# Kernel optimization log

Hardware: AMD Instinct MI355X
Metric: run time of the kernel (lower is better)

The kernel has to match this reference:

```python
import jax, jax.numpy as jnp
import numpy as np
import math

N_NODES = 16384
N_GRAPHS = 512
E2 = 65536
E3 = 393216
EMB = 300
SCH = 128
NG = 50
CUTOFF = 10.0
NL_GIN = 5
NL_SCH = 6
NTASK = 12


def _ssp(x):
    # ShiftedSoftplus used by SchNet
    return jax.nn.softplus(x) - math.log(2.0)


def _seg(x, ids, n):
    return jax.ops.segment_sum(x, ids, num_segments=n)


def _forward(x2d, edge_index_2d, edge_attr_2d, batch, z, pos, edge_index_3d,
             atom_emb1, atom_emb2, vn_init,
             gin_W1, gin_b1, gin_W2, gin_b2, gin_bond1, gin_bond2, gin_gamma, gin_beta,
             vn_W1, vn_b1, vn_W2, vn_b2,
             sch_emb, s_mW1, s_mb1, s_mW2, s_mb2, s_lin1W, s_lin2W, s_lin2b, s_linW, s_linb,
             p2W, p2b, p3W, p3b, gW1, gb1, gW2, gb2, cW1, cb1, cW2, cb2):
    counts = jnp.maximum(_seg(jnp.ones((N_NODES,), jnp.float32), batch, N_GRAPHS), 1.0)[:, None]
    # ---------- GIN (2D) encoder with virtual node (OGB-style, eval mode: dropout off, BN uses running stats 0/1) ----------
    src2, dst2 = edge_index_2d[0], edge_index_2d[1]
    h = atom_emb1[x2d[:, 0]] + atom_emb2[x2d[:, 1]]              # [N, 300]
    vn = jnp.broadcast_to(vn_init, (N_GRAPHS, EMB))
    for l in range(NL_GIN):
        h_in = h + vn[batch]
        eemb = gin_bond1[l][edge_attr_2d[:, 0]] + gin_bond2[l][edge_attr_2d[:, 1]]
        msg = jax.nn.relu(h_in[src2] + eemb)                     # [E2, 300]
        agg = _seg(msg, dst2, N_NODES)
        t = jax.nn.relu((h_in + agg) @ gin_W1[l] + gin_b1[l]) @ gin_W2[l] + gin_b2[l]
        t = t * gin_gamma[l] + gin_beta[l]                       # eval-mode BatchNorm
        if l < NL_GIN - 1:
            t = jax.nn.relu(t)
            vn_tmp = _seg(t, batch, N_GRAPHS) + vn
            vn = jax.nn.relu(jax.nn.relu(vn_tmp @ vn_W1[l] + vn_b1[l]) @ vn_W2[l] + vn_b2[l])
        h = t
    h2d = _seg(h, batch, N_GRAPHS) / counts                      # global_mean_pool
    # ---------- SchNet (3D) encoder: interaction layers only, residual additions ----------
    src3, dst3 = edge_index_3d[0], edge_index_3d[1]
    diff = pos[dst3] - pos[src3]
    d = jnp.sqrt(jnp.sum(diff * diff, axis=-1))                  # edge_weight [E3]; no self loops -> d > 0
    offsets = jnp.linspace(0.0, CUTOFF, NG)
    coeff = -0.5 / (offsets[1] - offsets[0]) ** 2
    rbf = jnp.exp(coeff * (d[:, None] - offsets) ** 2)           # GaussianSmearing [E3, 50]
    C = 0.5 * (jnp.cos(d * math.pi / CUTOFF) + 1.0)              # cosine cutoff
    hs = sch_emb[z]                                              # [N, 128]
    for l in range(NL_SCH):
        Wf = (_ssp(rbf @ s_mW1[l] + s_mb1[l]) @ s_mW2[l] + s_mb2[l]) * C[:, None]  # filter net [E3, 128]
        x1 = hs @ s_lin1W[l]                                     # CFConv lin1 (no bias)
        agg = _seg(x1[src3] * Wf, dst3, N_NODES)                 # continuous-filter conv
        x2 = agg @ s_lin2W[l] + s_lin2b[l]                       # CFConv lin2
        hs = hs + (_ssp(x2) @ s_linW[l] + s_linb[l])             # block act+lin, residual
    h3d = _seg(hs, batch, N_GRAPHS) / counts
    # ---------- gated fusion + classifier (dropout off in eval) ----------
    h2p = h2d @ p2W + p2b
    h3p = h3d @ p3W + p3b
    g = jax.nn.sigmoid(jax.nn.relu(jnp.concatenate([h2p, h3p], axis=1) @ gW1 + gb1) @ gW2 + gb2)  # [B, 1]
    hf = g * h2p + (1.0 - g) * h3p
    return jax.nn.relu(hf @ cW1 + cb1) @ cW2 + cb2               # [N_GRAPHS, NTASK]


def setup_inputs() -> dict:
    key = jax.random.key(0)
    ks = jax.random.split(key, 40)
    def r(i, shape, s=0.02):
        return jax.random.normal(ks[i], shape, dtype=jnp.float32) * s
    x2d = jax.random.randint(ks[0], (N_NODES, 2), 0, 3)
    src2 = jax.random.randint(ks[1], (E2,), 0, N_NODES)
    dst2 = (src2 + jax.random.randint(ks[2], (E2,), 1, N_NODES)) % N_NODES  # no self loops
    edge_index_2d = jnp.stack([src2, dst2])
    edge_attr_2d = jax.random.randint(ks[3], (E2, 2), 0, 3)
    batch = jnp.sort(jax.random.randint(ks[4], (N_NODES,), 0, N_GRAPHS))
    z = jax.random.randint(ks[5], (N_NODES,), 0, 100)
    pos = jax.random.normal(ks[6], (N_NODES, 3), dtype=jnp.float32) * 2.0
    src3 = jax.random.randint(ks[7], (E3,), 0, N_NODES)
    dst3 = (src3 + jax.random.randint(ks[8], (E3,), 1, N_NODES)) % N_NODES
    edge_index_3d = jnp.stack([src3, dst3])
    return dict(
        x2d=x2d, edge_index_2d=edge_index_2d, edge_attr_2d=edge_attr_2d, batch=batch,
        z=z, pos=pos, edge_index_3d=edge_index_3d,
        atom_emb1=r(9, (120, EMB)), atom_emb2=r(10, (3, EMB)),
        vn_init=jnp.zeros((EMB,), jnp.float32),
        gin_W1=r(11, (NL_GIN, EMB, 2 * EMB)), gin_b1=jnp.zeros((NL_GIN, 2 * EMB), jnp.float32),
        gin_W2=r(12, (NL_GIN, 2 * EMB, EMB)), gin_b2=jnp.zeros((NL_GIN, EMB), jnp.float32),
        gin_bond1=r(13, (NL_GIN, 6, EMB)), gin_bond2=r(14, (NL_GIN, 3, EMB)),
        gin_gamma=jnp.ones((NL_GIN, EMB), jnp.float32), gin_beta=jnp.zeros((NL_GIN, EMB), jnp.float32),
        vn_W1=r(15, (NL_GIN - 1, EMB, 2 * EMB)), vn_b1=jnp.zeros((NL_GIN - 1, 2 * EMB), jnp.float32),
        vn_W2=r(16, (NL_GIN - 1, 2 * EMB, EMB)), vn_b2=jnp.zeros((NL_GIN - 1, EMB), jnp.float32),
        sch_emb=r(17, (100, SCH), 0.1),
        s_mW1=r(18, (NL_SCH, NG, SCH), 0.1), s_mb1=jnp.zeros((NL_SCH, SCH), jnp.float32),
        s_mW2=r(19, (NL_SCH, SCH, SCH), 0.1), s_mb2=jnp.zeros((NL_SCH, SCH), jnp.float32),
        s_lin1W=r(20, (NL_SCH, SCH, SCH), 0.1),
        s_lin2W=r(21, (NL_SCH, SCH, SCH), 0.1), s_lin2b=jnp.zeros((NL_SCH, SCH), jnp.float32),
        s_linW=r(22, (NL_SCH, SCH, SCH), 0.1), s_linb=jnp.zeros((NL_SCH, SCH), jnp.float32),
        p2W=r(23, (EMB, EMB)), p2b=jnp.zeros((EMB,), jnp.float32),
        p3W=r(24, (SCH, EMB)), p3b=jnp.zeros((EMB,), jnp.float32),
        gW1=r(25, (2 * EMB, 128)), gb1=jnp.zeros((128,), jnp.float32),
        gW2=r(26, (128, 1)), gb2=jnp.zeros((1,), jnp.float32),
        cW1=r(27, (EMB, EMB // 2)), cb1=jnp.zeros((EMB // 2,), jnp.float32),
        cW2=r(28, (EMB // 2, NTASK)), cb2=jnp.zeros((NTASK,), jnp.float32),
    )


def reference(x2d, edge_index_2d, edge_attr_2d, batch, z, pos, edge_index_3d,
              atom_emb1, atom_emb2, vn_init,
              gin_W1, gin_b1, gin_W2, gin_b2, gin_bond1, gin_bond2, gin_gamma, gin_beta,
              vn_W1, vn_b1, vn_W2, vn_b2,
              sch_emb, s_mW1, s_mb1, s_mW2, s_mb2, s_lin1W, s_lin2W, s_lin2b, s_linW, s_linb,
              p2W, p2b, p3W, p3b, gW1, gb1, gW2, gb2, cW1, cb1, cW2, cb2):
    return _forward(x2d, edge_index_2d, edge_attr_2d, batch, z, pos, edge_index_3d,
                    atom_emb1, atom_emb2, vn_init,
                    gin_W1, gin_b1, gin_W2, gin_b2, gin_bond1, gin_bond2, gin_gamma, gin_beta,
                    vn_W1, vn_b1, vn_W2, vn_b2,
                    sch_emb, s_mW1, s_mb1, s_mW2, s_mb2, s_lin1W, s_lin2W, s_lin2b, s_linW, s_linb,
                    p2W, p2b, p3W, p3b, gW1, gb1, gW2, gb2, cW1, cb1, cW2, cb2)
```

## Files before the change

### kernel.cpp

```cpp
#include <hip/hip_runtime.h>
#include <hip/hip_bf16.h>
#include <math.h>

#define NN 16384
#define NG 512
#define NE2 65536
#define NE3 393216
#define DEMB 300
#define DSCH 128
#define NRBF 50
#define NTAB 5120
#define TROWS 5121
#define DMAX 25.0f

typedef __attribute__((ext_vector_type(8))) short bf16x8;
typedef __attribute__((ext_vector_type(4))) float f32x4;

__device__ __forceinline__ float sspf(float x) {
  float sp = log1pf(expf(-fabsf(x))) + fmaxf(x, 0.f);
  return sp - 0.69314718055994530942f;
}

__device__ __forceinline__ short f2b(float f) {
  union { float f; unsigned u; } v;
  v.f = f;
  unsigned r = v.u + 0x7FFF + ((v.u >> 16) & 1);
  return (short)(r >> 16);
}

__device__ __forceinline__ float b2f(unsigned short b) {
  union { unsigned u; float f; } v;
  v.u = ((unsigned)b) << 16;
  return v.f;
}


__global__ void k_hist3(const int* __restrict__ ei2, const int* __restrict__ ei3,
                        const int* __restrict__ batch, int* __restrict__ cnt2,
                        int* __restrict__ cnt3, int* __restrict__ cntg) {
  int i = blockIdx.x * blockDim.x + threadIdx.x;
  if (i < NE2) {
    atomicAdd(&cnt2[ei2[NE2 + i]], 1);
  } else if (i < NE2 + NE3) {
    atomicAdd(&cnt3[ei3[NE3 + (i - NE2)]], 1);
  } else if (i < NE2 + NE3 + NN) {
    atomicAdd(&cntg[batch[i - NE2 - NE3]], 1);
  }
}

__global__ __launch_bounds__(1024) void k_scan3(const int* __restrict__ c0, int* __restrict__ o0,
                                                int n0, const int* __restrict__ c1,
                                                int* __restrict__ o1, int n1,
                                                const int* __restrict__ c2, int* __restrict__ o2,
                                                int n2) {
  const int* cnt = (blockIdx.x == 0) ? c0 : (blockIdx.x == 1) ? c1 : c2;
  int* off = (blockIdx.x == 0) ? o0 : (blockIdx.x == 1) ? o1 : o2;
  int n = (blockIdx.x == 0) ? n0 : (blockIdx.x == 1) ? n1 : n2;
  __shared__ int part[1024];
  int tid = threadIdx.x;
  int per = (n + 1023) / 1024;
  int base = tid * per;
  int sum = 0;
  for (int i = 0; i < per; ++i) {
    int idx = base + i;
    if (idx < n) sum += cnt[idx];
  }
  part[tid] = sum;
  __syncthreads();
  for (int d = 1; d < 1024; d <<= 1) {
    int v = (tid >= d) ? part[tid - d] : 0;
    __syncthreads();
    part[tid] += v;
    __syncthreads();
  }
  int run = (tid == 0) ? 0 : part[tid - 1];
  for (int i = 0; i < per; ++i) {
    int idx = base + i;
    if (idx < n) {
      off[idx] = run;
      run += cnt[idx];
    }
  }
  if (tid == 0) off[n] = part[1023];
}

__global__ void k_scatterB(const int* __restrict__ ei2, const int* __restrict__ ea2,
                           const int* __restrict__ batch, const int* __restrict__ off2,
                           int* __restrict__ cur2, int* __restrict__ s2s, int* __restrict__ ec2s,
                           int* __restrict__ b2s, const int* __restrict__ ei3,
                           const float* __restrict__ pos, const int* __restrict__ off3,
                           int* __restrict__ cur3, int* __restrict__ s3s, int* __restrict__ id3s,
                           float* __restrict__ fr3s) {
  int i = blockIdx.x * blockDim.x + threadIdx.x;
  if (i < NE2) {
    int e = i;
    int s = ei2[e], d = ei2[NE2 + e];
    int p = atomicAdd(&cur2[d], 1);
    int j = off2[d] + p;
    s2s[j] = s;
    ec2s[j] = ea2[2 * e] * 4 + ea2[2 * e + 1];
    b2s[j] = batch[s];
  } else if (i < NE2 + NE3) {
    int e = i - NE2;
    int s = ei3[e], d = ei3[NE3 + e];
    float dx = pos[3 * d] - pos[3 * s];
    float dy = pos[3 * d + 1] - pos[3 * s + 1];
    float dz = pos[3 * d + 2] - pos[3 * s + 2];
    float dist = sqrtf(dx * dx + dy * dy + dz * dz);
    float u = fminf(dist * ((float)NTAB / DMAX), (float)NTAB - 0.001f);
    int idx = (int)u;
    int p = atomicAdd(&cur3[d], 1);
    int j = off3[d] + p;
    s3s[j] = s;
    id3s[j] = idx;
    fr3s[j] = u - (float)idx;
  }
}


__global__ void k_init_gin(const int* __restrict__ x2d, const float* __restrict__ e1,
                           const float* __restrict__ e2, short* __restrict__ hb,
                           const float* __restrict__ vni, float* __restrict__ vn,
                           short* __restrict__ vnb) {
  int i = blockIdx.x * blockDim.x + threadIdx.x;
  if (i < NN * DEMB) {
    int n = i / DEMB, c = i - n * DEMB;
    hb[i] = f2b(e1[x2d[2 * n] * DEMB + c] + e2[x2d[2 * n + 1] * DEMB + c]);
  } else if (i < NN * DEMB + NG * DEMB) {
    int j = i - NN * DEMB;
    float v = vni[j % DEMB];
    vn[j] = v;
    vnb[j] = f2b(v);
  }
}

__global__ void k_init_sch(float* __restrict__ rbs, float* __restrict__ Cs,
                           const int* __restrict__ z, const float* __restrict__ emb,
                           float* __restrict__ hs, short* __restrict__ hsb) {
  int i = blockIdx.x * blockDim.x + threadIdx.x;
  if (i < TROWS * NRBF) {
    int j = i / NRBF, k = i - j * NRBF;
    float dj = (float)j * (DMAX / (float)NTAB);
    const float step = 10.0f / 49.0f;
    const float coeff = -0.5f / (step * step);
    float t = dj - (float)k * step;
    rbs[i] = expf(coeff * t * t);
    if (k == 0) Cs[j] = 0.5f * (cosf(dj * (3.14159265358979323846f / 10.0f)) + 1.0f);
  } else if (i < TROWS * NRBF + NN * DSCH) {
    int j = i - TROWS * NRBF;
    float v = emb[z[j >> 7] * DSCH + (j & 127)];
    hs[j] = v;
    hsb[j] = f2b(v);
  }
}

__global__ __launch_bounds__(256) void k_head5(
    const float* __restrict__ h2d, const float* __restrict__ h3d, const float* __restrict__ p2W,
    const float* __restrict__ p2b, const float* __restrict__ p3W, const float* __restrict__ p3b,
    const float* __restrict__ gW1, const float* __restrict__ gb1, const float* __restrict__ gW2,
    const float* __restrict__ gb2, const float* __restrict__ cW1, const float* __restrict__ cb1,
    const float* __restrict__ cW2, const float* __restrict__ cb2, float* __restrict__ out) {
  __shared__ float sx[DEMB], sy[DSCH], h2p[DEMB], h3p[DEMB], ghl[DSCH], c1l[150];
  __shared__ float pa[2][128], pb[2][128];
  __shared__ float gshare;
  int g = blockIdx.x, tid = threadIdx.x;
  int half = tid >> 7, o7 = tid & 127;
  for (int i = tid; i < DEMB; i += 256) sx[i] = h2d[(size_t)g * DEMB + i];
  if (tid < DSCH) sy[tid] = h3d[(size_t)g * DSCH + tid];
  __syncthreads();
  for (int ob = 0; ob < DEMB; ob += 128) {
    int o = ob + o7;
    float a0 = 0.f, a1 = 0.f, b0 = 0.f, b1 = 0.f;
    if (o < DEMB) {
      int kb = half * 150;
      for (int k = kb; k < kb + 150; k += 2) {
        a0 = fmaf(sx[k], p2W[k * 300 + o], a0);
        a1 = fmaf(sx[k + 1], p2W[(k + 1) * 300 + o], a1);
      }
      int kb3 = half * 64;
      for (int k = kb3; k < kb3 + 64; k += 2) {
        b0 = fmaf(sy[k], p3W[k * 300 + o], b0);
        b1 = fmaf(sy[k + 1], p3W[(k + 1) * 300 + o], b1);
      }
    }
    pa[half][o7] = a0 + a1;
    pb[half][o7] = b0 + b1;
    __syncthreads();
    if (half == 0 && o < DEMB) {
      h2p[o] = pa[0][o7] + pa[1][o7] + p2b[o];
      h3p[o] = pb[0][o7] + pb[1][o7] + p3b[o];
    }
    __syncthreads();
  }
  {
    const float* src = (half == 0) ? h2p : h3p;
    const float* wb = gW1 + (half ? 300 * 128 : 0);
    float a0 = 0.f, a1 = 0.f, a2 = 0.f, a3 = 0.f;
    for (int k = 0; k < 300; k += 4) {
      a0 = fmaf(src[k], wb[k * 128 + o7], a0);
      a1 = fmaf(src[k + 1], wb[(k + 1) * 128 + o7], a1);
      a2 = fmaf(src[k + 2], wb[(k + 2) * 128 + o7], a2);
      a3 = fmaf(src[k + 3], wb[(k + 3) * 128 + o7], a3);
    }
    pa[half][o7] = (a0 + a1) + (a2 + a3);
    __syncthreads();
    if (half == 0) ghl[o7] = fmaxf(pa[0][o7] + pa[1][o7] + gb1[o7], 0.f);
    __syncthreads();
  }
  if (tid < 128) pa[0][tid] = ghl[tid] * gW2[tid];
  __syncthreads();
  for (int s = 64; s > 0; s >>= 1) {
    if (tid < s) pa[0][tid] += pa[0][tid + s];
    __syncthreads();
  }
  if (tid == 0) gshare = 1.0f / (1.0f + expf(-(pa[0][0] + gb2[0])));
  __syncthreads();
  float gg = gshare;
  for (int i = tid; i < DEMB; i += 256) sx[i] = gg * h2p[i] + (1.0f - gg) * h3p[i];
  __syncthreads();
  for (int ob = 0; ob < 150; ob += 128) {
    int o = ob + o7;
    float a0 = 0.f, a1 = 0.f;
    if (o < 150) {
      int kb = half * 150;
      for (int k = kb; k < kb + 150; k += 2) {
        a0 = fmaf(sx[k], cW1[k * 150 + o], a0);
        a1 = fmaf(sx[k + 1], cW1[(k + 1) * 150 + o], a1);
      }
    }
    pa[half][o7] = a0 + a1;
    __syncthreads();
    if (half == 0 && o < 150) c1l[o] = fmaxf(pa[0][o7] + pa[1][o7] + cb1[o], 0.f);
    __syncthreads();
  }
  if (tid < 12) {
    float a = cb2[tid];
    for (int k = 0; k < 150; ++k) a = fmaf(c1l[k], cW2[k * 12 + tid], a);
    out[(size_t)g * 12 + tid] = a;
  }
}


__global__ __launch_bounds__(256) void k_gin_gather4(
    const short* __restrict__ hb, const short* __restrict__ vnb, const int* __restrict__ batch,
    const int* __restrict__ off2, const int* __restrict__ s2s, const int* __restrict__ ec2s,
    const int* __restrict__ b2s, const float* __restrict__ bond1,
    const float* __restrict__ bond2, short* __restrict__ aggb) {
  __shared__ float sb[9 * DEMB];
  int tid = threadIdx.x;
  for (int i = tid; i < 6 * DEMB; i += 256) sb[i] = bond1[i];
  for (int i = tid; i < 3 * DEMB; i += 256) sb[6 * DEMB + i] = bond2[i];
  __syncthreads();
  int d = blockIdx.x * 4 + (tid >> 6);
  int lane = tid & 63;
  int j0 = off2[d], j1 = off2[d + 1];
  const unsigned short* hd = (const unsigned short*)hb + (size_t)d * DEMB;
  const unsigned short* vd = (const unsigned short*)vnb + (size_t)batch[d] * DEMB;
  float acc[5];
#pragma unroll
  for (int q = 0; q < 5; ++q) {
    int col = lane + 64 * q;
    acc[q] = (col < DEMB) ? b2f(hd[col]) + b2f(vd[col]) : 0.f;
  }
  for (int j = j0; j < j1; ++j) {
    int s = s2s[j], ec = ec2s[j], bs = b2s[j];
    const unsigned short* hr = (const unsigned short*)hb + (size_t)s * DEMB;
    const unsigned short* vr = (const unsigned short*)vnb + (size_t)bs * DEMB;
    const float* b1 = sb + (ec >> 2) * DEMB;
    const float* b2 = sb + 6 * DEMB + (ec & 3) * DEMB;
#pragma unroll
    for (int q = 0; q < 5; ++q) {
      int col = lane + 64 * q;
      if (col < DEMB) acc[q] += fmaxf(b2f(hr[col]) + b2f(vr[col]) + b1[col] + b2[col], 0.f);
    }
  }
  short* outr = aggb + (size_t)d * 320;
#pragma unroll
  for (int q = 0; q < 5; ++q) {
    int col = lane + 64 * q;
    outr[col] = (col < DEMB) ? f2b(acc[q]) : (short)0;
  }
}

__global__ __launch_bounds__(256) void k_conv_gather4(
    const short* __restrict__ ftabb, const short* __restrict__ x1b, const int* __restrict__ off3,
    const int* __restrict__ s3s, const int* __restrict__ id3s, const float* __restrict__ fr3s,
    short* __restrict__ agg3b) {
  int tid = threadIdx.x;
  int d = blockIdx.x * 4 + (tid >> 6);
  int lane = tid & 63;
  int j0 = off3[d], j1 = off3[d + 1];
  float a0 = 0.f, a1 = 0.f;
  for (int j = j0; j < j1; ++j) {
    int s = s3s[j], idx = id3s[j];
    float fr = fr3s[j];
    unsigned t0 = ((const unsigned*)(ftabb + (size_t)idx * 128))[lane];
    unsigned t1 = ((const unsigned*)(ftabb + (size_t)(idx + 1) * 128))[lane];
    unsigned xv = ((const unsigned*)(x1b + (size_t)s * 128))[lane];
    float t0a = b2f((unsigned short)(t0 & 0xFFFF)), t0b = b2f((unsigned short)(t0 >> 16));
    float t1a = b2f((unsigned short)(t1 & 0xFFFF)), t1b = b2f((unsigned short)(t1 >> 16));
    a0 += (t0a + fr * (t1a - t0a)) * b2f((unsigned short)(xv & 0xFFFF));
    a1 += (t0b + fr * (t1b - t0b)) * b2f((unsigned short)(xv >> 16));
  }
  unsigned pack = ((unsigned)(unsigned short)f2b(a1) << 16) | (unsigned short)f2b(a0);
  ((unsigned*)(agg3b + (size_t)d * 128))[lane] = pack;
}

__global__ __launch_bounds__(256) void k_poolb300(const short* __restrict__ xb,
                                                  const int* __restrict__ goff,
                                                  float* __restrict__ out) {
  int g = blockIdx.x * 4 + (threadIdx.x >> 6);
  int lane = threadIdx.x & 63;
  if (g >= NG) return;
  int r0 = goff[g], r1 = goff[g + 1];
  float acc[5] = {};
  for (int r = r0; r < r1; ++r) {
    const unsigned short* row = (const unsigned short*)xb + (size_t)r * DEMB;
#pragma unroll
    for (int q = 0; q < 5; ++q) {
      int col = lane + 64 * q;
      if (col < DEMB) acc[q] += b2f(row[col]);
    }
  }
  float s = 1.0f / fmaxf((float)(r1 - r0), 1.0f);
#pragma unroll
  for (int q = 0; q < 5; ++q) {
    int col = lane + 64 * q;
    if (col < DEMB) out[(size_t)g * DEMB + col] = acc[q] * s;
  }
}

__global__ __launch_bounds__(256) void k_poolb128(const short* __restrict__ xb,
                                                  const int* __restrict__ goff,
                                                  float* __restrict__ out) {
  int g = blockIdx.x * 4 + (threadIdx.x >> 6);
  int lane = threadIdx.x & 63;
  if (g >= NG) return;
  int r0 = goff[g], r1 = goff[g + 1];
  float a0 = 0.f, a1 = 0.f;
  for (int r = r0; r < r1; ++r) {
    unsigned v = ((const unsigned*)(xb + (size_t)r * DSCH))[lane];
    a0 += b2f((unsigned short)(v & 0xFFFF));
    a1 += b2f((unsigned short)(v >> 16));
  }
  float s = 1.0f / fmaxf((float)(r1 - r0), 1.0f);
  out[(size_t)g * DSCH + lane * 2] = a0 * s;
  out[(size_t)g * DSCH + lane * 2 + 1] = a1 * s;
}

__global__ __launch_bounds__(256) void k_poolvn(const short* __restrict__ hb,
                                                const int* __restrict__ goff,
                                                const float* __restrict__ vn,
                                                short* __restrict__ vnab) {
  int g = blockIdx.x * 4 + (threadIdx.x >> 6);
  int lane = threadIdx.x & 63;
  if (g >= NG) return;
  int r0 = goff[g], r1 = goff[g + 1];
  float acc[5] = {};
  for (int r = r0; r < r1; ++r) {
    const unsigned short* row = (const unsigned short*)hb + (size_t)r * DEMB;
#pragma unroll
    for (int q = 0; q < 5; ++q) {
      int col = lane + 64 * q;
      if (col < DEMB) acc[q] += b2f(row[col]);
    }
  }
  short* outr = vnab + (size_t)g * 320;
#pragma unroll
  for (int q = 0; q < 5; ++q) {
    int col = lane + 64 * q;
    if (col < 320)
      outr[col] = (col < DEMB) ? f2b(acc[q] + vn[(size_t)g * DEMB + col]) : (short)0;
  }
}

__global__ void k_prepw2(const float* __restrict__ Wa, const float* __restrict__ Wb,
                         short* __restrict__ Wta, short* __restrict__ Wtb, int K, int N, int Kp,
                         int Np, int La, int Lb) {
  int i = blockIdx.x * blockDim.x + threadIdx.x;
  int per = Np * Kp;
  if (i >= (La + Lb) * per) return;
  int l = i / per, r = i - l * per;
  int n = r / Kp, k = r - n * Kp;
  const float* W = (l < La) ? Wa : Wb;
  int ll = (l < La) ? l : l - La;
  short* Wt = (l < La) ? Wta : Wtb;
  float v = (n < N && k < K) ? W[(size_t)ll * K * N + (size_t)k * N + n] : 0.f;
  Wt[(size_t)ll * per + r] = f2b(v);
}

__global__ void k_prepw3(const float* __restrict__ W0, const float* __restrict__ W1,
                         const float* __restrict__ W2, short* __restrict__ T0,
                         short* __restrict__ T1, short* __restrict__ T2) {
  int i = blockIdx.x * blockDim.x + threadIdx.x;
  const int per = 6 * 128 * 128;
  if (i >= 3 * per) return;
  int which = i / per, r = i - which * per;
  int l = r / 16384, rr = r - l * 16384;
  int n = rr / 128, k = rr - n * 128;
  const float* W = (which == 0) ? W0 : (which == 1) ? W1 : W2;
  short* T = (which == 0) ? T0 : (which == 1) ? T1 : T2;
  T[r] = f2b(W[(size_t)l * 16384 + (size_t)k * 128 + n]);
}

template <int ACT>
__global__ __launch_bounds__(256) void k_gemmz(
    const float* __restrict__ A, const float* __restrict__ B, const float* __restrict__ bias,
    const float* __restrict__ rscale, float* __restrict__ Cout, short* __restrict__ Coutb,
    int M, int N, int K, int ldc, long strideA, long strideB, long strideBias, long strideC) {
  A += (size_t)blockIdx.z * strideA;
  B += (size_t)blockIdx.z * strideB;
  bias += (size_t)blockIdx.z * strideBias;
  __shared__ float sA[16][65];
  __shared__ float sB[16][64];
  int tid = threadIdx.x;
  int tx = tid & 15, ty = tid >> 4;
  int bm = blockIdx.y * 64, bn = blockIdx.x * 64;
  float acc[4][4] = {};
  for (int k0 = 0; k0 < K; k0 += 16) {
#pragma unroll
    for (int t = 0; t < 4; ++t) {
      int i = tid + t * 256;
      int m = i >> 4, kk = i & 15;
      int gm = bm + m, gk = k0 + kk;
      sA[kk][m] = (gm < M && gk < K) ? A[(size_t)gm * K + gk] : 0.f;
    }
#pragma unroll
    for (int t = 0; t < 4; ++t) {
      int i = tid + t * 256;
      int kk = i >> 6, n = i & 63;
      int gk = k0 + kk, gn = bn + n;
      sB[kk][n] = (gk < K && gn < N) ? B[(size_t)gk * N + gn] : 0.f;
    }
    __syncthreads();
#pragma unroll
    for (int kk = 0; kk < 16; ++kk) {
      float a[4], b[4];
#pragma unroll
      for (int i = 0; i < 4; ++i) a[i] = sA[kk][ty + 16 * i];
#pragma unroll
      for (int j = 0; j < 4; ++j) b[j] = sB[kk][tx + 16 * j];
#pragma unroll
      for (int i = 0; i < 4; ++i)
#pragma unroll
        for (int j = 0; j < 4; ++j) acc[i][j] = fmaf(a[i], b[j], acc[i][j]);
    }
    __syncthreads();
  }
#pragma unroll
  for (int i = 0; i < 4; ++i) {
    int gm = bm + ty + 16 * i;
    if (gm >= M) continue;
    float rs = rscale ? rscale[gm] : 1.0f;
#pragma unroll
    for (int j = 0; j < 4; ++j) {
      int gn = bn + tx + 16 * j;
      if (gn >= N) continue;
      float v = acc[i][j] + bias[gn];
      if (ACT == 1) v = fmaxf(v, 0.f);
      if (ACT == 2) v = sspf(v);
      v *= rs;
      if (Cout) Cout[(size_t)blockIdx.z * strideC + (size_t)gm * ldc + gn] = v;
      if (Coutb) Coutb[(size_t)blockIdx.z * strideC + (size_t)gm * ldc + gn] = f2b(v);
    }
  }
}

template <int ACT>
__global__ __launch_bounds__(256) void k_mgemm_bf(
    const short* __restrict__ Ab, const short* __restrict__ Wt, const float* __restrict__ bias,
    const float* __restrict__ scale, const float* __restrict__ shift,
    const float* __restrict__ Cin, float* __restrict__ Cout, short* __restrict__ Coutb,
    int M, int N, int Kp, int ldc, int ldcb, int Nb) {
  __shared__ short sA[128 * 32];
  const int tid = threadIdx.x;
  const int lane = tid & 63;
  const int w = tid >> 6;
  const int wm = w >> 1, wn = w & 1;
  const int bm = blockIdx.y * 128, bn = blockIdx.x * 128;

  f32x4 acc[4][4] = {};

  const int sr = tid >> 1;
  const int sk = (tid & 1) * 16;
  const short* Arow = Ab + (size_t)(bm + sr) * Kp + sk;
// ... 304 lines not shown
                              int out_size, void* d_ws, size_t ws_size, hipStream_t stream) {
  const int* x2d = (const int*)d_in[0];
  const int* ei2 = (const int*)d_in[1];
  const int* ea2 = (const int*)d_in[2];
  const int* batch = (const int*)d_in[3];
  const int* z = (const int*)d_in[4];
  const float* pos = (const float*)d_in[5];
  const int* ei3 = (const int*)d_in[6];
  const float* atom_emb1 = (const float*)d_in[7];
  const float* atom_emb2 = (const float*)d_in[8];
  const float* vn_init = (const float*)d_in[9];
  const float* gin_W1 = (const float*)d_in[10];
  const float* gin_b1 = (const float*)d_in[11];
  const float* gin_W2 = (const float*)d_in[12];
  const float* gin_b2 = (const float*)d_in[13];
  const float* gin_bond1 = (const float*)d_in[14];
  const float* gin_bond2 = (const float*)d_in[15];
  const float* gin_gamma = (const float*)d_in[16];
  const float* gin_beta = (const float*)d_in[17];
  const float* vn_W1 = (const float*)d_in[18];
  const float* vn_b1 = (const float*)d_in[19];
  const float* vn_W2 = (const float*)d_in[20];
  const float* vn_b2 = (const float*)d_in[21];
  const float* sch_emb = (const float*)d_in[22];
  const float* s_mW1 = (const float*)d_in[23];
  const float* s_mb1 = (const float*)d_in[24];
  const float* s_mW2 = (const float*)d_in[25];
  const float* s_mb2 = (const float*)d_in[26];
  const float* s_lin1W = (const float*)d_in[27];
  const float* s_lin2W = (const float*)d_in[28];
  const float* s_lin2b = (const float*)d_in[29];
  const float* s_linW = (const float*)d_in[30];
  const float* s_linb = (const float*)d_in[31];
  const float* p2W = (const float*)d_in[32];
  const float* p2b = (const float*)d_in[33];
  const float* p3W = (const float*)d_in[34];
  const float* p3b = (const float*)d_in[35];
  const float* gW1 = (const float*)d_in[36];
  const float* gb1 = (const float*)d_in[37];
  const float* gW2 = (const float*)d_in[38];
  const float* gb2 = (const float*)d_in[39];
  const float* cW1 = (const float*)d_in[40];
  const float* cb1 = (const float*)d_in[41];
  const float* cW2 = (const float*)d_in[42];
  const float* cb2 = (const float*)d_in[43];

  float* ws = (float*)d_ws;
  short* hb = (short*)ws;
  int* b2s = (int*)(ws + 2500000);
  short* aggb = (short*)(ws + 5000000);
  short* y1b = (short*)(ws + 7700000);
  float* rbs = ws + 400000;
  float* Cs = ws + 700000;
  float* t1all = ws + 800000;
  short* ftabb = (short*)(ws + 4800000);
  float* hs = ws + 8800000;
  short* x1b = (short*)(ws + 11000000);
  short* agg3b = (short*)(ws + 13200000);
  short* hsb = (short*)(ws + 15400000);
  short* W1t = (short*)(ws + 20000000);
  short* W2t = (short*)(ws + 20600000);
  short* s1t = (short*)(ws + 21200000);
  short* s2t = (short*)(ws + 21300000);
  short* s3t = (short*)(ws + 21400000);
  int* I = (int*)(ws + 22000000);
  int* cnt2 = I + 0;
  int* cnt3 = I + 16384;
  int* cntg = I + 32768;
  int* cur2 = I + 33280;
  int* cur3 = I + 49664;
  int* off2 = I + 70000;
  int* off3 = I + 90000;
  int* goff = I + 110000;
  int* s2s = I + 120000;
  int* ec2s = I + 190000;
  int* s3s = I + 260000;
  int* id3s = I + 660000;
  float* fr3s = (float*)(I + 1060000);
  short* vnW1t = (short*)(ws + 23500000);
  short* vnW2t = (short*)(ws + 24000000);
  short* vnab = (short*)(ws + 24500000);
  short* vnhb = (short*)(ws + 24600000);
  short* vnb = (short*)(ws + 24800000);
  float* vn = ws + 28443136;
  float* h2d = ws + 29057536;
  float* h3d = ws + 29211136;

  k_prepw2<<<(9 * 640 * 320 + 255) / 256, 256, 0, stream>>>(gin_W1, vn_W1, W1t, vnW1t, 300, 600,
                                                            320, 640, 5, 4);
  k_prepw2<<<(9 * 384 * 608 + 255) / 256, 256, 0, stream>>>(gin_W2, vn_W2, W2t, vnW2t, 600, 300,
                                                            608, 384, 5, 4);
  k_prepw3<<<(3 * 6 * 16384 + 255) / 256, 256, 0, stream>>>(s_lin1W, s_lin2W, s_linW, s1t, s2t,
                                                            s3t);

  hipMemsetAsync(I, 0, 66048 * sizeof(int), stream);
  k_hist3<<<(NE2 + NE3 + NN + 255) / 256, 256, 0, stream>>>(ei2, ei3, batch, cnt2, cnt3, cntg);
  k_scan3<<<3, 1024, 0, stream>>>(cnt2, off2, 16384, cnt3, off3, 16384, cntg, goff, 512);
  k_scatterB<<<(NE2 + NE3 + 255) / 256, 256, 0, stream>>>(ei2, ea2, batch, off2, cur2, s2s, ec2s,
                                                          b2s, ei3, pos, off3, cur3, s3s, id3s,
                                                          fr3s);

  k_init_gin<<<(NN * DEMB + NG * DEMB + 255) / 256, 256, 0, stream>>>(x2d, atom_emb1, atom_emb2,
                                                                      hb, vn_init, vn, vnb);
  for (int l = 0; l < 5; ++l) {
    k_gin_gather4<<<NN / 4, 256, 0, stream>>>(hb, vnb, batch, off2, s2s, ec2s, b2s,
                                              gin_bond1 + l * 6 * DEMB, gin_bond2 + l * 3 * DEMB,
                                              aggb);
    run_mgemm_bf(stream, aggb, W1t + (size_t)l * 640 * 320, gin_b1 + l * 600, nullptr, nullptr,
                 nullptr, nullptr, y1b, NN, 600, 320, 0, 608, 608, 1);
    run_mgemm_bf(stream, y1b, W2t + (size_t)l * 384 * 608, gin_b2 + l * 300, gin_gamma + l * 300,
                 gin_beta + l * 300, nullptr, nullptr, hb, NN, 300, 608, 0, 300, 300,
                 (l < 4) ? 1 : 0);
    if (l < 4) {
      k_poolvn<<<NG / 4, 256, 0, stream>>>(hb, goff, vn, vnab);
      run_mgemm_bf64(stream, vnab, vnW1t + (size_t)l * 640 * 320, vn_b1 + l * 600, nullptr,
                     nullptr, nullptr, nullptr, vnhb, NG, 600, 320, 0, 608, 608, 1);
      run_mgemm_bf64(stream, vnhb, vnW2t + (size_t)l * 384 * 608, vn_b2 + l * 300, nullptr,
                     nullptr, nullptr, vn, vnb, NG, 300, 608, 300, 300, 300, 1);
    }
  }
  k_poolb300<<<NG / 4, 256, 0, stream>>>(hb, goff, h2d);

  k_init_sch<<<(TROWS * NRBF + NN * DSCH + 255) / 256, 256, 0, stream>>>(rbs, Cs, z, sch_emb, hs,
                                                                         hsb);
  {
    dim3 ga(2, (TROWS + 63) / 64, 6);
    k_gemmz<2><<<ga, 256, 0, stream>>>(rbs, s_mW1, s_mb1, nullptr, t1all, nullptr, TROWS, 128, 50,
                                       128, 0L, 50L * 128, 128L, (long)TROWS * 128);
    k_gemmz<0><<<ga, 256, 0, stream>>>(t1all, s_mW2, s_mb2, Cs, nullptr, ftabb, TROWS, 128, 128,
                                       128, (long)TROWS * 128, 128L * 128, 128L,
                                       (long)TROWS * 128);
  }
  run_mgemm_bf64(stream, hsb, s1t, nullptr, nullptr, nullptr, nullptr, nullptr, x1b, NN, 128, 128,
                 0, 128, 128, 0);
  for (int l = 0; l < 6; ++l) {
    k_conv_gather4<<<NN / 4, 256, 0, stream>>>(ftabb + (size_t)l * TROWS * 128, x1b, off3, s3s,
                                               id3s, fr3s, agg3b);
    if (l < 5)
      k_sch_fused<0><<<NN / 64, 256, 0, stream>>>(agg3b, s2t + (size_t)l * 16384,
                                                  s_lin2b + l * 128, s3t + (size_t)l * 16384,
                                                  s_linb + l * 128, s1t + (size_t)(l + 1) * 16384,
                                                  hs, hsb, x1b);
    else
      k_sch_fused<1><<<NN / 64, 256, 0, stream>>>(agg3b, s2t + (size_t)l * 16384,
                                                  s_lin2b + l * 128, s3t + (size_t)l * 16384,
                                                  s_linb + l * 128, s1t, hs, hsb, x1b);
  }
  k_poolb128<<<NG / 4, 256, 0, stream>>>(hsb, goff, h3d);

  k_head5<<<NG, 256, 0, stream>>>(h2d, h3d, p2W, p2b, p3W, p3b, gW1, gb1, gW2, gb2, cW1, cb1, cW2,
                                  cb2, (float*)d_out);
}
```

Before: 1.349 ms.

## Replace scalar head kernel with bf16 matrix GEMMs and vectorize gathers

The per-graph scalar head kernel is replaced by a chain of bf16 matrix-core GEMMs over concatenated, padded weight matrices, with a small blend kernel for the gate. Pooling now writes bf16 into a shared concatenated input buffer. Separately, the GIN gather is rewritten to load packed bf16 pairs as 32-bit words and to pre-sum the two bond embeddings into a combined bf16 table in shared memory. This adds bf16 rounding of head weights and bond sums, plus an extra weight-prep launch.

```diff
diff --git a/kernel.cpp b/kernel.cpp
--- a/kernel.cpp
+++ b/kernel.cpp
@@ -32,6 +32,10 @@
   union { unsigned u; float f; } v;
   v.u = ((unsigned)b) << 16;
   return v.f;
+}
+
+__device__ __forceinline__ unsigned pk2(float a, float b) {
+  return ((unsigned)(unsigned short)f2b(b) << 16) | (unsigned short)f2b(a);
 }
 
 
@@ -154,132 +158,69 @@
   }
 }
 
-__global__ __launch_bounds__(256) void k_head5(
-    const float* __restrict__ h2d, const float* __restrict__ h3d, const float* __restrict__ p2W,
-    const float* __restrict__ p2b, const float* __restrict__ p3W, const float* __restrict__ p3b,
-    const float* __restrict__ gW1, const float* __restrict__ gb1, const float* __restrict__ gW2,
-    const float* __restrict__ gb2, const float* __restrict__ cW1, const float* __restrict__ cb1,
-    const float* __restrict__ cW2, const float* __restrict__ cb2, float* __restrict__ out) {
-  __shared__ float sx[DEMB], sy[DSCH], h2p[DEMB], h3p[DEMB], ghl[DSCH], c1l[150];
-  __shared__ float pa[2][128], pb[2][128];
-  __shared__ float gshare;
-  int g = blockIdx.x, tid = threadIdx.x;
-  int half = tid >> 7, o7 = tid & 127;
-  for (int i = tid; i < DEMB; i += 256) sx[i] = h2d[(size_t)g * DEMB + i];
-  if (tid < DSCH) sy[tid] = h3d[(size_t)g * DSCH + tid];
-  __syncthreads();
-  for (int ob = 0; ob < DEMB; ob += 128) {
-    int o = ob + o7;
-    float a0 = 0.f, a1 = 0.f, b0 = 0.f, b1 = 0.f;
-    if (o < DEMB) {
-      int kb = half * 150;
-      for (int k = kb; k < kb + 150; k += 2) {
-        a0 = fmaf(sx[k], p2W[k * 300 + o], a0);
-        a1 = fmaf(sx[k + 1], p2W[(k + 1) * 300 + o], a1);
-      }
-      int kb3 = half * 64;
-      for (int k = kb3; k < kb3 + 64; k += 2) {
-        b0 = fmaf(sy[k], p3W[k * 300 + o], b0);
-        b1 = fmaf(sy[k + 1], p3W[(k + 1) * 300 + o], b1);
-      }
-    }
-    pa[half][o7] = a0 + a1;
-    pb[half][o7] = b0 + b1;
-    __syncthreads();
-    if (half == 0 && o < DEMB) {
-      h2p[o] = pa[0][o7] + pa[1][o7] + p2b[o];
-      h3p[o] = pb[0][o7] + pb[1][o7] + p3b[o];
-    }
-    __syncthreads();
-  }
-  {
-    const float* src = (half == 0) ? h2p : h3p;
-    const float* wb = gW1 + (half ? 300 * 128 : 0);
-    float a0 = 0.f, a1 = 0.f, a2 = 0.f, a3 = 0.f;
-    for (int k = 0; k < 300; k += 4) {
-      a0 = fmaf(src[k], wb[k * 128 + o7], a0);
-      a1 = fmaf(src[k + 1], wb[(k + 1) * 128 + o7], a1);
-      a2 = fmaf(src[k + 2], wb[(k + 2) * 128 + o7], a2);
-      a3 = fmaf(src[k + 3], wb[(k + 3) * 128 + o7], a3);
-    }
-    pa[half][o7] = (a0 + a1) + (a2 + a3);
-    __syncthreads();
-    if (half == 0) ghl[o7] = fmaxf(pa[0][o7] + pa[1][o7] + gb1[o7], 0.f);
-    __syncthreads();
-  }
-  if (tid < 128) pa[0][tid] = ghl[tid] * gW2[tid];
-  __syncthreads();
-  for (int s = 64; s > 0; s >>= 1) {
-    if (tid < s) pa[0][tid] += pa[0][tid + s];
-    __syncthreads();
-  }
-  if (tid == 0) gshare = 1.0f / (1.0f + expf(-(pa[0][0] + gb2[0])));
-  __syncthreads();
-  float gg = gshare;
-  for (int i = tid; i < DEMB; i += 256) sx[i] = gg * h2p[i] + (1.0f - gg) * h3p[i];
-  __syncthreads();
-  for (int ob = 0; ob < 150; ob += 128) {
-    int o = ob + o7;
-    float a0 = 0.f, a1 = 0.f;
-    if (o < 150) {
-      int kb = half * 150;
-      for (int k = kb; k < kb + 150; k += 2) {
-        a0 = fmaf(sx[k], cW1[k * 150 + o], a0);
-        a1 = fmaf(sx[k + 1], cW1[(k + 1) * 150 + o], a1);
-      }
-    }
-    pa[half][o7] = a0 + a1;
-    __syncthreads();
-    if (half == 0 && o < 150) c1l[o] = fmaxf(pa[0][o7] + pa[1][o7] + cb1[o], 0.f);
-    __syncthreads();
-  }
-  if (tid < 12) {
-    float a = cb2[tid];
-    for (int k = 0; k < 150; ++k) a = fmaf(c1l[k], cW2[k * 12 + tid], a);
-    out[(size_t)g * 12 + tid] = a;
-  }
-}
-
-
-__global__ __launch_bounds__(256) void k_gin_gather4(
+
+__global__ __launch_bounds__(256) void k_gin_gather5(
     const short* __restrict__ hb, const short* __restrict__ vnb, const int* __restrict__ batch,
     const int* __restrict__ off2, const int* __restrict__ s2s, const int* __restrict__ ec2s,
     const int* __restrict__ b2s, const float* __restrict__ bond1,
     const float* __restrict__ bond2, short* __restrict__ aggb) {
-  __shared__ float sb[9 * DEMB];
+  __shared__ unsigned sb[18 * 150];
   int tid = threadIdx.x;
-  for (int i = tid; i < 6 * DEMB; i += 256) sb[i] = bond1[i];
-  for (int i = tid; i < 3 * DEMB; i += 256) sb[6 * DEMB + i] = bond2[i];
+  for (int i = tid; i < 18 * 150; i += 256) {
+    int c = i / 150, u = i - c * 150;
+    int a0 = c / 3, a1 = c - a0 * 3;
+    float v0 = bond1[a0 * 300 + 2 * u] + bond2[a1 * 300 + 2 * u];
+    float v1 = bond1[a0 * 300 + 2 * u + 1] + bond2[a1 * 300 + 2 * u + 1];
+    sb[i] = pk2(v0, v1);
+  }
   __syncthreads();
   int d = blockIdx.x * 4 + (tid >> 6);
-  int lane = tid & 63;
+  int l = tid & 63;
   int j0 = off2[d], j1 = off2[d + 1];
-  const unsigned short* hd = (const unsigned short*)hb + (size_t)d * DEMB;
-  const unsigned short* vd = (const unsigned short*)vnb + (size_t)batch[d] * DEMB;
-  float acc[5];
-#pragma unroll
-  for (int q = 0; q < 5; ++q) {
-    int col = lane + 64 * q;
-    acc[q] = (col < DEMB) ? b2f(hd[col]) + b2f(vd[col]) : 0.f;
+  const unsigned* hu = (const unsigned*)hb + (size_t)d * 150;
+  const unsigned* vu = (const unsigned*)vnb + (size_t)batch[d] * 150;
+  const int u0 = l, u1 = l + 64, u2 = l + 128;
+  const bool has2 = (u2 < 150);
+  float acc[6];
+  {
+    unsigned a = hu[u0], b = vu[u0];
+    acc[0] = b2f((unsigned short)a) + b2f((unsigned short)b);
+    acc[1] = b2f((unsigned short)(a >> 16)) + b2f((unsigned short)(b >> 16));
+    a = hu[u1]; b = vu[u1];
+    acc[2] = b2f((unsigned short)a) + b2f((unsigned short)b);
+    acc[3] = b2f((unsigned short)(a >> 16)) + b2f((unsigned short)(b >> 16));
+    if (has2) {
+      a = hu[u2]; b = vu[u2];
+      acc[4] = b2f((unsigned short)a) + b2f((unsigned short)b);
+      acc[5] = b2f((unsigned short)(a >> 16)) + b2f((unsigned short)(b >> 16));
+    } else {
+      acc[4] = acc[5] = 0.f;
+    }
   }
   for (int j = j0; j < j1; ++j) {
     int s = s2s[j], ec = ec2s[j], bs = b2s[j];
-    const unsigned short* hr = (const unsigned short*)hb + (size_t)s * DEMB;
-    const unsigned short* vr = (const unsigned short*)vnb + (size_t)bs * DEMB;
-    const float* b1 = sb + (ec >> 2) * DEMB;
-    const float* b2 = sb + 6 * DEMB + (ec & 3) * DEMB;
-#pragma unroll
-    for (int q = 0; q < 5; ++q) {
-      int col = lane + 64 * q;
-      if (col < DEMB) acc[q] += fmaxf(b2f(hr[col]) + b2f(vr[col]) + b1[col] + b2[col], 0.f);
-    }
-  }
-  short* outr = aggb + (size_t)d * 320;
-#pragma unroll
-  for (int q = 0; q < 5; ++q) {
-    int col = lane + 64 * q;
-    outr[col] = (col < DEMB) ? f2b(acc[q]) : (short)0;
-  }
+    const unsigned* hr = (const unsigned*)hb + (size_t)s * 150;
+    const unsigned* vr = (const unsigned*)vnb + (size_t)bs * 150;
+    const unsigned* eu = sb + ((ec >> 2) * 3 + (ec & 3)) * 150;
+    unsigned a = hr[u0], b = vr[u0], e = eu[u0];
+    acc[0] += fmaxf(b2f((unsigned short)a) + b2f((unsigned short)b) + b2f((unsigned short)e), 0.f);
+    acc[1] += fmaxf(b2f((unsigned short)(a >> 16)) + b2f((unsigned short)(b >> 16)) +
+                        b2f((unsigned short)(e >> 16)), 0.f);
+    a = hr[u1]; b = vr[u1]; e = eu[u1];
+    acc[2] += fmaxf(b2f((unsigned short)a) + b2f((unsigned short)b) + b2f((unsigned short)e), 0.f);
+    acc[3] += fmaxf(b2f((unsigned short)(a >> 16)) + b2f((unsigned short)(b >> 16)) +
+                        b2f((unsigned short)(e >> 16)), 0.f);
+    if (has2) {
+      a = hr[u2]; b = vr[u2]; e = eu[u2];
+      acc[4] += fmaxf(b2f((unsigned short)a) + b2f((unsigned short)b) + b2f((unsigned short)e), 0.f);
+      acc[5] += fmaxf(b2f((unsigned short)(a >> 16)) + b2f((unsigned short)(b >> 16)) +
+                          b2f((unsigned short)(e >> 16)), 0.f);
+    }
+  }
+  unsigned* outu = (unsigned*)aggb + (size_t)d * 160;
+  outu[u0] = pk2(acc[0], acc[1]);
+  outu[u1] = pk2(acc[2], acc[3]);
+  if (u2 < 160) outu[u2] = has2 ? pk2(acc[4], acc[5]) : 0u;
 }
 
 __global__ __launch_bounds__(256) void k_conv_gather4(
@@ -302,50 +243,7 @@
     a0 += (t0a + fr * (t1a - t0a)) * b2f((unsigned short)(xv & 0xFFFF));
     a1 += (t0b + fr * (t1b - t0b)) * b2f((unsigned short)(xv >> 16));
   }
-  unsigned pack = ((unsigned)(unsigned short)f2b(a1) << 16) | (unsigned short)f2b(a0);
-  ((unsigned*)(agg3b + (size_t)d * 128))[lane] = pack;
-}
-
-__global__ __launch_bounds__(256) void k_poolb300(const short* __restrict__ xb,
-                                                  const int* __restrict__ goff,
-                                                  float* __restrict__ out) {
-  int g = blockIdx.x * 4 + (threadIdx.x >> 6);
-  int lane = threadIdx.x & 63;
-  if (g >= NG) return;
-  int r0 = goff[g], r1 = goff[g + 1];
-  float acc[5] = {};
-  for (int r = r0; r < r1; ++r) {
-    const unsigned short* row = (const unsigned short*)xb + (size_t)r * DEMB;
-#pragma unroll
-    for (int q = 0; q < 5; ++q) {
-      int col = lane + 64 * q;
-      if (col < DEMB) acc[q] += b2f(row[col]);
-    }
-  }
-  float s = 1.0f / fmaxf((float)(r1 - r0), 1.0f);
-#pragma unroll
-  for (int q = 0; q < 5; ++q) {
-    int col = lane + 64 * q;
-    if (col < DEMB) out[(size_t)g * DEMB + col] = acc[q] * s;
-  }
-}
-
-__global__ __launch_bounds__(256) void k_poolb128(const short* __restrict__ xb,
-                                                  const int* __restrict__ goff,
-                                                  float* __restrict__ out) {
-  int g = blockIdx.x * 4 + (threadIdx.x >> 6);
-  int lane = threadIdx.x & 63;
-  if (g >= NG) return;
-  int r0 = goff[g], r1 = goff[g + 1];
-  float a0 = 0.f, a1 = 0.f;
-  for (int r = r0; r < r1; ++r) {
-    unsigned v = ((const unsigned*)(xb + (size_t)r * DSCH))[lane];
-    a0 += b2f((unsigned short)(v & 0xFFFF));
-    a1 += b2f((unsigned short)(v >> 16));
-  }
-  float s = 1.0f / fmaxf((float)(r1 - r0), 1.0f);
-  out[(size_t)g * DSCH + lane * 2] = a0 * s;
-  out[(size_t)g * DSCH + lane * 2 + 1] = a1 * s;
+  ((unsigned*)(agg3b + (size_t)d * 128))[lane] = pk2(a0, a1);
 }
 
 __global__ __launch_bounds__(256) void k_poolvn(const short* __restrict__ hb,
@@ -353,24 +251,116 @@
                                                 const float* __restrict__ vn,
                                                 short* __restrict__ vnab) {
   int g = blockIdx.x * 4 + (threadIdx.x >> 6);
-  int lane = threadIdx.x & 63;
+  int l = threadIdx.x & 63;
   if (g >= NG) return;
   int r0 = goff[g], r1 = goff[g + 1];
-  float acc[5] = {};
+  const int u0 = l, u1 = l + 64, u2 = l + 128;
+  const bool has2 = (u2 < 150);
+  float acc[6] = {};
   for (int r = r0; r < r1; ++r) {
-    const unsigned short* row = (const unsigned short*)hb + (size_t)r * DEMB;
-#pragma unroll
-    for (int q = 0; q < 5; ++q) {
-      int col = lane + 64 * q;
-      if (col < DEMB) acc[q] += b2f(row[col]);
-    }
-  }
-  short* outr = vnab + (size_t)g * 320;
-#pragma unroll
-  for (int q = 0; q < 5; ++q) {
-    int col = lane + 64 * q;
-    if (col < 320)
-      outr[col] = (col < DEMB) ? f2b(acc[q] + vn[(size_t)g * DEMB + col]) : (short)0;
+    const unsigned* hu = (const unsigned*)hb + (size_t)r * 150;
+    unsigned a = hu[u0];
+    acc[0] += b2f((unsigned short)a);
+    acc[1] += b2f((unsigned short)(a >> 16));
+    a = hu[u1];
+    acc[2] += b2f((unsigned short)a);
+    acc[3] += b2f((unsigned short)(a >> 16));
+    if (has2) {
+      a = hu[u2];
+      acc[4] += b2f((unsigned short)a);
+      acc[5] += b2f((unsigned short)(a >> 16));
+    }
+  }
+  const float2* v2 = (const float2*)(vn + (size_t)g * 300);
+  unsigned* outu = (unsigned*)vnab + (size_t)g * 160;
+  float2 w = v2[u0];
+  outu[u0] = pk2(acc[0] + w.x, acc[1] + w.y);
+  w = v2[u1];
+  outu[u1] = pk2(acc[2] + w.x, acc[3] + w.y);
+  if (u2 < 160) {
+    if (has2) {
+      w = v2[u2];
+      outu[u2] = pk2(acc[4] + w.x, acc[5] + w.y);
+    } else {
+      outu[u2] = 0u;
+    }
+  }
+}
+
+__global__ __launch_bounds__(256) void k_poolhead2(const short* __restrict__ hb,
+                                                   const int* __restrict__ goff,
+                                                   short* __restrict__ xcat) {
+  int g = blockIdx.x * 4 + (threadIdx.x >> 6);
+  int l = threadIdx.x & 63;
+  if (g >= NG) return;
+  int r0 = goff[g], r1 = goff[g + 1];
+  const int u0 = l, u1 = l + 64, u2 = l + 128;
+  const bool has2 = (u2 < 150);
+  float acc[6] = {};
+  for (int r = r0; r < r1; ++r) {
+    const unsigned* hu = (const unsigned*)hb + (size_t)r * 150;
+    unsigned a = hu[u0];
+    acc[0] += b2f((unsigned short)a);
+    acc[1] += b2f((unsigned short)(a >> 16));
+    a = hu[u1];
+    acc[2] += b2f((unsigned short)a);
+    acc[3] += b2f((unsigned short)(a >> 16));
+    if (has2) {
+      a = hu[u2];
+      acc[4] += b2f((unsigned short)a);
+      acc[5] += b2f((unsigned short)(a >> 16));
+    }
+  }
+  float s = 1.0f / fmaxf((float)(r1 - r0), 1.0f);
+  unsigned* outu = (unsigned*)xcat + (size_t)g * 224;
+  outu[u0] = pk2(acc[0] * s, acc[1] * s);
+  outu[u1] = pk2(acc[2] * s, acc[3] * s);
+  if (u2 < 160) outu[u2] = has2 ? pk2(acc[4] * s, acc[5] * s) : 0u;
+}
+
+__global__ __launch_bounds__(256) void k_poolhead3(const short* __restrict__ hsb,
+                                                   const int* __restrict__ goff,
+                                                   short* __restrict__ xcat) {
+  int g = blockIdx.x * 4 + (threadIdx.x >> 6);
+  int l = threadIdx.x & 63;
+  if (g >= NG) return;
+  int r0 = goff[g], r1 = goff[g + 1];
+  float a0 = 0.f, a1 = 0.f;
+  for (int r = r0; r < r1; ++r) {
+    unsigned v = ((const unsigned*)hsb)[(size_t)r * 64 + l];
+    a0 += b2f((unsigned short)(v & 0xFFFF));
+    a1 += b2f((unsigned short)(v >> 16));
+  }
+  float s = 1.0f / fmaxf((float)(r1 - r0), 1.0f);
+  ((unsigned*)xcat)[(size_t)g * 224 + 160 + l] = pk2(a0 * s, a1 * s);
+}
+
+__global__ __launch_bounds__(256) void k_blend(const float* __restrict__ gh,
+                                               const float* __restrict__ gW2,
+                                               const float* __restrict__ gb2,
+                                               const float* __restrict__ hcat,
+                                               short* __restrict__ hfb) {
+  int g = blockIdx.x * 4 + (threadIdx.x >> 6);
+  int l = threadIdx.x & 63;
+  if (g >= NG) return;
+  float2 v = ((const float2*)(gh + (size_t)g * 128))[l];
+  float dot = v.x * gW2[2 * l] + v.y * gW2[2 * l + 1];
+  for (int m = 32; m; m >>= 1) dot += __shfl_xor(dot, m);
+  float gg = 1.0f / (1.0f + expf(-(dot + gb2[0])));
+  const float* hc = hcat + (size_t)g * 608;
+  unsigned* outu = (unsigned*)hfb + (size_t)g * 160;
+  const int u0 = l, u1 = l + 64, u2 = l + 128;
+  float a0 = hc[2 * u0], a1 = hc[2 * u0 + 1], b0 = hc[304 + 2 * u0], b1 = hc[304 + 2 * u0 + 1];
+  outu[u0] = pk2(gg * a0 + (1.f - gg) * b0, gg * a1 + (1.f - gg) * b1);
+  a0 = hc[2 * u1]; a1 = hc[2 * u1 + 1]; b0 = hc[304 + 2 * u1]; b1 = hc[304 + 2 * u1 + 1];
+  outu[u1] = pk2(gg * a0 + (1.f - gg) * b0, gg * a1 + (1.f - gg) * b1);
+  if (u2 < 160) {
+    if (u2 < 150) {
+      a0 = hc[2 * u2]; a1 = hc[2 * u2 + 1]; b0 = hc[304 + 2 * u2]; b1 = hc[304 + 2 * u2 + 1];
+      outu[u2] = pk2(gg * a0 + (1.f - gg) * b0, gg * a1 + (1.f - gg) * b1);
+    } else {
+      outu[u2] = 0u;
+    }
   }
 }
 
@@ -401,6 +391,48 @@
   const float* W = (which == 0) ? W0 : (which == 1) ? W1 : W2;
   short* T = (which == 0) ? T0 : (which == 1) ? T1 : T2;
   T[r] = f2b(W[(size_t)l * 16384 + (size_t)k * 128 + n]);
+}
+
+#define W1SZ (608 * 448)
+#define G1SZ (128 * 608)
+#define C1SZ (160 * 320)
+#define C2SZ (12 * 160)
+__global__ void k_prephead(const float* __restrict__ p2W, const float* __restrict__ p2b,
+                           const float* __restrict__ p3W, const float* __restrict__ p3b,
+                           const float* __restrict__ gW1, const float* __restrict__ cW1,
+                           const float* __restrict__ cb1, const float* __restrict__ cW2,
+                           short* __restrict__ Wcat, short* __restrict__ gW1cat,
+                           short* __restrict__ cW1cat, short* __restrict__ cW2cat,
+                           float* __restrict__ bcat, float* __restrict__ cb1p) {
+  int i = blockIdx.x * blockDim.x + threadIdx.x;
+  if (i < W1SZ) {
+    int o = i / 448, k = i - o * 448;
+    float v = 0.f;
+    if (o < 300 && k < 300) v = p2W[(size_t)k * 300 + o];
+    else if (o >= 304 && o < 604 && k >= 320) v = p3W[(size_t)(k - 320) * 300 + (o - 304)];
+    Wcat[i] = f2b(v);
+  } else if (i < W1SZ + G1SZ) {
+    int r = i - W1SZ;
+    int o = r / 608, k = r - o * 608;
+    float v = 0.f;
+    if (k < 300) v = gW1[(size_t)k * 128 + o];
+    else if (k >= 304 && k < 604) v = gW1[(size_t)(300 + k - 304) * 128 + o];
+    gW1cat[r] = f2b(v);
+  } else if (i < W1SZ + G1SZ + C1SZ) {
+    int r = i - W1SZ - G1SZ;
+    int o = r / 320, k = r - o * 320;
+    cW1cat[r] = f2b((o < 150 && k < 300) ? cW1[(size_t)k * 150 + o] : 0.f);
+  } else if (i < W1SZ + G1SZ + C1SZ + C2SZ) {
+    int r = i - W1SZ - G1SZ - C1SZ;
+    int o = r / 160, k = r - o * 160;
+    cW2cat[r] = f2b((k < 150) ? cW2[(size_t)k * 12 + o] : 0.f);
+  } else if (i < W1SZ + G1SZ + C1SZ + C2SZ + 608) {
+    int o = i - W1SZ - G1SZ - C1SZ - C2SZ;
+    bcat[o] = (o < 300) ? p2b[o] : (o >= 304 && o < 604) ? p3b[o - 304] : 0.f;
+  } else if (i < W1SZ + G1SZ + C1SZ + C2SZ + 608 + 160) {
+    int o = i - W1SZ - G1SZ - C1SZ - C2SZ - 608;
+    cb1p[o] = (o < 150) ? cb1[o] : 0.f;
+  }
 }
 
 template <int ACT>
@@ -871,9 +903,19 @@
   short* vnab = (short*)(ws + 24500000);
   short* vnhb = (short*)(ws + 24600000);
   short* vnb = (short*)(ws + 24800000);
+  short* Wcat = (short*)(ws + 25000000);
+  short* gW1cat = (short*)(ws + 25200000);
+  short* cW1cat = (short*)(ws + 25250000);
+  short* cW2cat = (short*)(ws + 25280000);
+  float* bcat = ws + 25290000;
+  float* cb1p = ws + 25291000;
+  short* xcat = (short*)(ws + 25300000);
+  float* hcat = ws + 25430000;
+  short* hcatb = (short*)(ws + 25750000);
+  float* gh = ws + 25920000;
+  short* hfb = (short*)(ws + 26000000);
+  short* c1b = (short*)(ws + 26100000);
   float* vn = ws + 28443136;
-  float* h2d = ws + 29057536;
-  float* h3d = ws + 29211136;
 
   k_prepw2<<<(9 * 640 * 320 + 255) / 256, 256, 0, stream>>>(gin_W1, vn_W1, W1t, vnW1t, 300, 600,
                                                             320, 640, 5, 4);
@@ -881,6 +923,8 @@
                                                             608, 384, 5, 4);
   k_prepw3<<<(3 * 6 * 16384 + 255) / 256, 256, 0, stream>>>(s_lin1W, s_lin2W, s_linW, s1t, s2t,
                                                             s3t);
+  k_prephead<<<(W1SZ + G1SZ + C1SZ + C2SZ + 608 + 160 + 255) / 256, 256, 0, stream>>>(
+      p2W, p2b, p3W, p3b, gW1, cW1, cb1, cW2, Wcat, gW1cat, cW1cat, cW2cat, bcat, cb1p);
 
   hipMemsetAsync(I, 0, 66048 * sizeof(int), stream);
   k_hist3<<<(NE2 + NE3 + NN + 255) / 256, 256, 0, stream>>>(ei2, ei3, batch, cnt2, cnt3, cntg);
@@ -892,7 +936,7 @@
   k_init_gin<<<(NN * DEMB + NG * DEMB + 255) / 256, 256, 0, stream>>>(x2d, atom_emb1, atom_emb2,
                                                                       hb, vn_init, vn, vnb);
   for (int l = 0; l < 5; ++l) {
-    k_gin_gather4<<<NN / 4, 256, 0, stream>>>(hb, vnb, batch, off2, s2s, ec2s, b2s,
+    k_gin_gather5<<<NN / 4, 256, 0, stream>>>(hb, vnb, batch, off2, s2s, ec2s, b2s,
                                               gin_bond1 + l * 6 * DEMB, gin_bond2 + l * 3 * DEMB,
                                               aggb);
     run_mgemm_bf(stream, aggb, W1t + (size_t)l * 640 * 320, gin_b1 + l * 600, nullptr, nullptr,
@@ -908,7 +952,7 @@
                      nullptr, nullptr, vn, vnb, NG, 300, 608, 300, 300, 300, 1);
     }
   }
-  k_poolb300<<<NG / 4, 256, 0, stream>>>(hb, goff, h2d);
+  k_poolhead2<<<NG / 4, 256, 0, stream>>>(hb, goff, xcat);
 
   k_init_sch<<<(TROWS * NRBF + NN * DSCH + 255) / 256, 256, 0, stream>>>(rbs, Cs, z, sch_emb, hs,
                                                                          hsb);
@@ -935,8 +979,15 @@
                                                   s_lin2b + l * 128, s3t + (size_t)l * 16384,
                                                   s_linb + l * 128, s1t, hs, hsb, x1b);
   }
-  k_poolb128<<<NG / 4, 256, 0, stream>>>(hsb, goff, h3d);
-
-  k_head5<<<NG, 256, 0, stream>>>(h2d, h3d, p2W, p2b, p3W, p3b, gW1, gb1, gW2, gb2, cW1, cb1, cW2,
-                                  cb2, (float*)d_out);
-}
+  k_poolhead3<<<NG / 4, 256, 0, stream>>>(hsb, goff, xcat);
+
+  run_mgemm_bf64(stream, xcat, Wcat, bcat, nullptr, nullptr, nullptr, hcat, hcatb, NG, 608, 448,
+                 608, 608, 608, 0);
+  run_mgemm_bf64(stream, hcatb, gW1cat, gb1, nullptr, nullptr, nullptr, gh, nullptr, NG, 128, 608,
+                 128, 128, 0, 1);
+  k_blend<<<NG / 4, 256, 0, stream>>>(gh, gW2, gb2, hcat, hfb);
+  run_mgemm_bf64(stream, hfb, cW1cat, cb1p, nullptr, nullptr, nullptr, nullptr, c1b, NG, 160, 320,
+                 0, 160, 160, 1);
+  run_mgemm_bf64(stream, c1b, cW2cat, cb2, nullptr, nullptr, nullptr, (float*)d_out, nullptr, NG,
+                 12, 160, 12, 12, 0, 0);
+}
```

Result: faster. 1.318 ms (-2.3%).
